# Kernel optimization log

Measured on AMD Instinct MI355X. Metric: run time of the kernel, lower is better.

The kernel has to match this reference:

```python
import jax, jax.numpy as jnp
import numpy as np

N_U = 50000
N_I = 50000
E = 800000
E_LBL = 200000
D_IN = 128
HID = 256
OUT = 128


def setup_inputs() -> dict:
    key = jax.random.key(0)
    ks = jax.random.split(key, 32)
    def glorot(k, shp):
        fan = shp[0] + shp[1]
        return jax.random.uniform(k, shp, jnp.float32, -1.0, 1.0) * np.sqrt(6.0 / fan)
    inp = {
        'x_user': jax.random.normal(ks[0], (N_U, D_IN), jnp.float32),
        'x_item': jax.random.normal(ks[1], (N_I, D_IN), jnp.float32),
        'edge_ui': jax.random.randint(ks[2], (2, E), 0, N_U, jnp.int32),
        'edge_iu': jax.random.randint(ks[3], (2, E), 0, N_I, jnp.int32),
        'edge_lbl': jax.random.randint(ks[4], (2, E_LBL), 0, N_U, jnp.int32),
        # layer 0 SAGE params (src_dim=D_IN, dst_dim=D_IN)
        'w_msg_ui0': glorot(ks[5], (D_IN, HID)), 'b_ui0': jnp.zeros((HID,), jnp.float32), 'w_root_ui0': glorot(ks[6], (D_IN, HID)),
        'w_msg_iu0': glorot(ks[7], (D_IN, HID)), 'b_iu0': jnp.zeros((HID,), jnp.float32), 'w_root_iu0': glorot(ks[8], (D_IN, HID)),
        # layer 1 SAGE params (src_dim=HID, dst_dim=HID)
        'w_msg_ui1': glorot(ks[9], (HID, HID)), 'b_ui1': jnp.zeros((HID,), jnp.float32), 'w_root_ui1': glorot(ks[10], (HID, HID)),
        'w_msg_iu1': glorot(ks[11], (HID, HID)), 'b_iu1': jnp.zeros((HID,), jnp.float32), 'w_root_iu1': glorot(ks[12], (HID, HID)),
        # per-node-type output linears on JK concat (2*HID -> OUT)
        'w_lin_u': glorot(ks[13], (2 * HID, OUT)), 'b_lin_u': jnp.zeros((OUT,), jnp.float32),
        'w_lin_i': glorot(ks[14], (2 * HID, OUT)), 'b_lin_i': jnp.zeros((OUT,), jnp.float32),
    }
    return inp


def _sage(x_src, x_dst, edge, w_msg, b_msg, w_root):
    # PyG SAGEConv(aggr='mean'): lin_l(mean_{j in N(i)} x_src[j]) + lin_r(x_dst[i])
    src, dst = edge[0], edge[1]
    n_dst = x_dst.shape[0]
    agg = jax.ops.segment_sum(x_src[src], dst, num_segments=n_dst)          # [n_dst, d_src]
    cnt = jax.ops.segment_sum(jnp.ones((edge.shape[1],), x_src.dtype), dst, num_segments=n_dst)
    mean = agg / jnp.maximum(cnt, 1.0)[:, None]
    return mean @ w_msg + b_msg + x_dst @ w_root


def reference(x_user, x_item, edge_ui, edge_iu, edge_lbl,
              w_msg_ui0, b_ui0, w_root_ui0, w_msg_iu0, b_iu0, w_root_iu0,
              w_msg_ui1, b_ui1, w_root_ui1, w_msg_iu1, b_iu1, w_root_iu1,
              w_lin_u, b_lin_u, w_lin_i, b_lin_i):
    # ----- encode: 2 HeteroConv(SAGEConv) layers -----
    item0 = _sage(x_user, x_item, edge_ui, w_msg_ui0, b_ui0, w_root_ui0)    # user->item
    user0 = _sage(x_item, x_user, edge_iu, b_msg=b_iu0, w_msg=w_msg_iu0, x_src=None, x_dst=None, edge=None, w_root=None) if False else _sage(x_item, x_user, edge_iu, w_msg_iu0, b_iu0, w_root_iu0)  # item->user
    item1 = _sage(user0, item0, edge_ui, w_msg_ui1, b_ui1, w_root_ui1)
    user1 = _sage(item0, user0, edge_iu, w_msg_iu1, b_iu1, w_root_iu1)
    # ----- JumpingKnowledge 'cat' + per-node-type linear -----
    z_user = jnp.concatenate([user0, user1], axis=-1) @ w_lin_u + b_lin_u   # [N_U, OUT]
    z_item = jnp.concatenate([item0, item1], axis=-1) @ w_lin_i + b_lin_i   # [N_I, OUT]
    # ----- decode: dot product over candidate edges (user, buys, item) -----
    pred = jnp.sum(z_user[edge_lbl[0]] * z_item[edge_lbl[1]], axis=-1)      # [E_LBL]
    return pred
```

## Files before the change

kernel.cpp:

```cpp
#include <hip/hip_runtime.h>

#define NU 50000
#define NI 50000
#define NE 800000
#define NLBL 200000
#define DIN 128
#define HID 256
#define DOUT 128

#define NSLICE 64
#define SLICE_SZ 12500
#define HALF_N 25000

typedef unsigned short ushort_t;
typedef __attribute__((ext_vector_type(8))) short bf16x8;
typedef __attribute__((ext_vector_type(4))) float f32x4;

__device__ __forceinline__ float bf2f(unsigned int u_shifted) {
    union { unsigned int i; float f; } v;
    v.i = u_shifted;
    return v.f;
}
__device__ __forceinline__ float bf_lo(unsigned int u) { return bf2f(u << 16); }
__device__ __forceinline__ float bf_hi(unsigned int u) { return bf2f(u & 0xffff0000u); }
__device__ __forceinline__ ushort_t f2bf(float f) {
    union { float f; unsigned int i; } v;
    v.f = f;
    unsigned int r = (v.i + 0x7FFFu + ((v.i >> 16) & 1u)) >> 16;
    return (ushort_t)r;
}
__device__ __forceinline__ void load_lds16(const ushort_t* g, ushort_t* s) {
    __builtin_amdgcn_global_load_lds(
        (const __attribute__((address_space(1))) void*)g,
        (__attribute__((address_space(3))) void*)s, 16, 0, 0);
}

#define CVT_PER 782
#define CVT_B (2 * CVT_PER)
#define SA_B 512

struct PrepArgs {
    const float* xu; ushort_t* xbu; const float* xi; ushort_t* xbi;
    const float *wm_ui1, *wr_ui1, *wm_iu1, *wr_iu1, *lin_i, *lin_u;
    float *G_i, *S_i, *G_u, *S_u;
};

__global__ __launch_bounds__(256) void prep_kernel(PrepArgs a) {
    int b = blockIdx.x;
    int t = threadIdx.x;
    if (b < CVT_B) {
        int cb = b;
        int which = (cb >= CVT_PER);
        if (which) cb -= CVT_PER;
        const float4* in = (const float4*)(which ? a.xi : a.xu);
        uint2* outp = (uint2*)(which ? a.xbi : a.xbu);
        const int n4 = NU * DIN / 4;
#pragma unroll
        for (int k = 0; k < 8; ++k) {
            int i = cb * 2048 + k * 256 + t;
            if (i < n4) {
                float4 v = in[i];
                uint2 o;
                o.x = (unsigned int)f2bf(v.x) | ((unsigned int)f2bf(v.y) << 16);
                o.y = (unsigned int)f2bf(v.z) | ((unsigned int)f2bf(v.w) << 16);
                outp[i] = o;
            }
        }
    } else {
        int r2 = b - CVT_B;
        int which = r2 >> 7;
        int e = (r2 & 127) * 256 + t;
        int k = e >> 7, n = e & 127;
        const float* W = (which == 0) ? a.wm_ui1 : (which == 1) ? a.wr_ui1
                       : (which == 2) ? a.wm_iu1 : a.wr_iu1;
        const float* L = (which < 2) ? a.lin_i : a.lin_u;
        float* O = (which == 0) ? a.G_i : (which == 1) ? a.S_i
                 : (which == 2) ? a.G_u : a.S_u;
        float s = (which & 1) ? L[k * 128 + n] : 0.f;
#pragma unroll 4
        for (int j = 0; j < HID; ++j) s += W[k * HID + j] * L[(HID + j) * 128 + n];
        O[k * 128 + n] = s;
    }
}

struct Prep2Args {
    const float *wm_ui0, *wr_ui0, *wm_iu0, *wr_iu0;
    const float *G_i, *S_i, *G_u, *S_u;
    const float *b_ui0, *b_iu0, *b_ui1, *b_iu1, *lin_i, *lin_u, *bl_i, *bl_u;
    ushort_t *VT1_i, *VT2_i, *VT3_i, *VT1_u, *VT2_u, *VT3_u;
    float *bz_i, *bz_u;
};

__global__ __launch_bounds__(256) void prep2_kernel(Prep2Args a) {
    int b = blockIdx.x, t = threadIdx.x;
    if (b < 384) {
        int v = b >> 6;
        int e = (b & 63) * 256 + t;
        int k = e >> 7, n = e & 127;
        const float *A1, *X1, *A2 = nullptr, *X2 = nullptr;
        ushort_t* O;
        switch (v) {
            case 0: A1 = a.wm_ui0; X1 = a.S_i; A2 = a.wr_iu0; X2 = a.G_i; O = a.VT1_i; break;
            case 1: A1 = a.wr_ui0; X1 = a.S_i; O = a.VT2_i; break;
            case 2: A1 = a.wm_iu0; X1 = a.G_i; O = a.VT3_i; break;
            case 3: A1 = a.wm_iu0; X1 = a.S_u; A2 = a.wr_ui0; X2 = a.G_u; O = a.VT1_u; break;
            case 4: A1 = a.wr_iu0; X1 = a.S_u; O = a.VT2_u; break;
            default: A1 = a.wm_ui0; X1 = a.G_u; O = a.VT3_u; break;
        }
        float s = 0.f;
#pragma unroll 4
        for (int j = 0; j < HID; ++j) s += A1[k * HID + j] * X1[j * 128 + n];
        if (A2) {
#pragma unroll 4
            for (int j = 0; j < HID; ++j) s += A2[k * HID + j] * X2[j * 128 + n];
        }
        O[n * 128 + k] = f2bf(s);
    } else {
        if (t >= 128) return;
        int user = b - 384;
        int n = t;
        const float* S = user ? a.S_u : a.S_i;
        const float* G = user ? a.G_u : a.G_i;
        const float* b_own0 = user ? a.b_iu0 : a.b_ui0;
        const float* b_oth0 = user ? a.b_ui0 : a.b_iu0;
        const float* b_own1 = user ? a.b_iu1 : a.b_ui1;
        const float* lin = user ? a.lin_u : a.lin_i;
        const float* bl = user ? a.bl_u : a.bl_i;
        float* o = user ? a.bz_u : a.bz_i;
        float s = bl[n];
        for (int j = 0; j < HID; ++j)
            s += b_own0[j] * S[j * 128 + n] + b_oth0[j] * G[j * 128 + n] +
                 b_own1[j] * lin[(HID + j) * 128 + n];
        o[n] = s;
    }
}

__global__ __launch_bounds__(256) void hist_lds(const int* __restrict__ dui,
                                                const int* __restrict__ diu,
                                                ushort_t* __restrict__ cnt_s) {
    __shared__ unsigned int cnt[HALF_N / 2];
    int b = blockIdx.x, t = threadIdx.x;
    int g = b >> 7, s = (b >> 1) & 63, half = b & 1;
    for (int i = t; i < HALF_N / 2; i += 256) cnt[i] = 0;
    __syncthreads();
    const int* dst = g ? diu : dui;
    int hbase = half * HALF_N;
    int e0 = s * SLICE_SZ;
    for (int i = e0 + t; i < e0 + SLICE_SZ; i += 256) {
        int d = dst[i] - hbase;
        if ((unsigned)d < (unsigned)HALF_N)
            atomicAdd(&cnt[d >> 1], 1u << ((d & 1) * 16));
    }
    __syncthreads();
    unsigned int* outp = (unsigned int*)(cnt_s + ((size_t)(g * NSLICE + s)) * 50000 + hbase);
    for (int i = t; i < HALF_N / 2; i += 256) outp[i] = cnt[i];
}

__global__ __launch_bounds__(256) void sscan(ushort_t* __restrict__ cnt_s, int* __restrict__ totals) {
    int idx = blockIdx.x * 256 + threadIdx.x;
    if (idx == 0) totals[100000] = 2 * NE;
    if (idx >= 100000) return;
    int g = idx / 50000, node = idx - g * 50000;
    size_t base = (size_t)g * NSLICE * 50000 + node;
    int run = 0;
#pragma unroll 4
    for (int s = 0; s < NSLICE; ++s) {
        size_t o = base + (size_t)s * 50000;
        int c = cnt_s[o];
        cnt_s[o] = (ushort_t)run;
        run += c;
    }
    totals[idx] = run;
}

__global__ __launch_bounds__(256) void scan1(const int* __restrict__ d, int* __restrict__ part, int n) {
    __shared__ int wsum[4];
    int b = blockIdx.x, t = threadIdx.x;
    int i0 = b * 2048 + t * 8;
    int s = 0;
#pragma unroll
    for (int k = 0; k < 8; ++k) s += (i0 + k < n) ? d[i0 + k] : 0;
#pragma unroll
    for (int off = 32; off > 0; off >>= 1) s += __shfl_down(s, off, 64);
    if ((t & 63) == 0) wsum[t >> 6] = s;
    __syncthreads();
    if (t == 0) part[b] = wsum[0] + wsum[1] + wsum[2] + wsum[3];
}

__global__ __launch_bounds__(256) void scan3(int* __restrict__ d, const int* __restrict__ part,
                                             int n, int nb) {
    __shared__ int wsum[4];
    __shared__ int blockoff_sh;
    int b = blockIdx.x, t = threadIdx.x;
    int lane = t & 63, wv = t >> 6;
    if (t < 64) {
        int v = (t < nb) ? part[t] : 0;
        int incl = v;
#pragma unroll
        for (int off = 1; off < 64; off <<= 1) {
            int tv = __shfl_up(incl, off, 64);
            if (t >= off) incl += tv;
        }
        if (t == b) blockoff_sh = incl - v;
    }
    int i0 = b * 2048 + t * 8;
    int v[8];
    int tsum = 0;
#pragma unroll
    for (int k = 0; k < 8; ++k) {
        v[k] = (i0 + k < n) ? d[i0 + k] : 0;
        tsum += v[k];
    }
    int incl = tsum;
#pragma unroll
    for (int off = 1; off < 64; off <<= 1) {
        int tv = __shfl_up(incl, off, 64);
        if (lane >= off) incl += tv;
    }
    if (lane == 63) wsum[wv] = incl;
    __syncthreads();
    int woff = 0;
    for (int w = 0; w < wv; ++w) woff += wsum[w];
    int run = blockoff_sh + woff + (incl - tsum);
#pragma unroll
    for (int k = 0; k < 8; ++k) {
        if (i0 + k < n) d[i0 + k] = run;
        run += v[k];
    }
}

__global__ __launch_bounds__(256) void fill_lds(const int* __restrict__ eui,
                                                const int* __restrict__ eiu,
                                                const ushort_t* __restrict__ cnt_s,
                                                const int* __restrict__ rowstart,
                                                ushort_t* __restrict__ csr) {
    __shared__ unsigned int off[HALF_N / 2];
    int b = blockIdx.x, t = threadIdx.x;
    int g = b >> 7, s = (b >> 1) & 63, half = b & 1;
    const unsigned int* st =
        (const unsigned int*)(cnt_s + ((size_t)(g * NSLICE + s)) * 50000 + half * HALF_N);
    for (int i = t; i < HALF_N / 2; i += 256) off[i] = st[i];
    __syncthreads();
    const int* src = g ? eiu : eui;
    const int* dst = src + NE;
    const int* rs = rowstart + g * 50000;
    int hbase = half * HALF_N;
    int e0 = s * SLICE_SZ;
    for (int i = e0 + t; i < e0 + SLICE_SZ; i += 256) {
        int dd = dst[i];
        int d = dd - hbase;
        if ((unsigned)d < (unsigned)HALF_N) {
            unsigned old = atomicAdd(&off[d >> 1], 1u << ((d & 1) * 16));
            int rel = (int)((old >> ((d & 1) * 16)) & 0xffffu);
            csr[(size_t)rs[dd] + rel] = (ushort_t)src[i];
        }
    }
}

struct AggJob { const int* sp; const ushort_t* csr; const ushort_t* x; ushort_t* out; int n; };
struct AggJobs2 { AggJob j[2]; };

__global__ __launch_bounds__(256) void agg_din(AggJobs2 js) {
    AggJob jb = js.j[blockIdx.y];
    int wave = (int)((blockIdx.x * 256u + threadIdx.x) >> 6);
    int lane = threadIdx.x & 63;
    const int l = lane & 15;
    const int h = lane >> 4;
    int w4 = wave * 4;
    if (w4 >= jb.n) return;
    int w = w4 + h;
    int s0 = jb.sp[w];
    int s1 = jb.sp[w + 1];
    int cnt = s1 - s0;
    float sc = (cnt > 0) ? 1.0f / (float)cnt : 0.0f;
    int cmax = cnt;
    {
        int c1 = __shfl_xor(cmax, 16, 64); cmax = (cmax > c1) ? cmax : c1;
        int c2 = __shfl_xor(cmax, 32, 64); cmax = (cmax > c2) ? cmax : c2;
    }
    const uint4* xp = (const uint4*)jb.x;
    float f0 = 0.f, f1 = 0.f, f2 = 0.f, f3 = 0.f;
    float f4 = 0.f, f5 = 0.f, f6 = 0.f, f7 = 0.f;
#define ACC8(m, u)                                                     \
    f0 = fmaf(m, bf_lo(u.x), f0); f1 = fmaf(m, bf_hi(u.x), f1);        \
    f2 = fmaf(m, bf_lo(u.y), f2); f3 = fmaf(m, bf_hi(u.y), f3);        \
    f4 = fmaf(m, bf_lo(u.z), f4); f5 = fmaf(m, bf_hi(u.z), f5);        \
    f6 = fmaf(m, bf_lo(u.w), f6); f7 = fmaf(m, bf_hi(u.w), f7);
    for (int chunk = 0; chunk < cmax; chunk += 16) {
        int mh = cnt - chunk;
        int safe = (mh > 0) ? ((l < mh) ? l : mh - 1) : 0;
        int vidx = (int)jb.csr[s0 + chunk + safe];
        int mm = cmax - chunk;
        if (mm > 16) mm = 16;
        int j = 0;
        for (; j + 3 < mm; j += 4) {
            int i0 = __shfl(vidx, j, 16);
            int i1 = __shfl(vidx, j + 1, 16);
            int i2 = __shfl(vidx, j + 2, 16);
            int i3 = __shfl(vidx, j + 3, 16);
            float m0 = (j < mh) ? 1.f : 0.f;
            float m1 = (j + 1 < mh) ? 1.f : 0.f;
            float m2 = (j + 2 < mh) ? 1.f : 0.f;
            float m3 = (j + 3 < mh) ? 1.f : 0.f;
            uint4 u0 = xp[(size_t)((j < mh) ? i0 : 0) * 16 + l];
            uint4 u1 = xp[(size_t)((j + 1 < mh) ? i1 : 0) * 16 + l];
            uint4 u2 = xp[(size_t)((j + 2 < mh) ? i2 : 0) * 16 + l];
            uint4 u3 = xp[(size_t)((j + 3 < mh) ? i3 : 0) * 16 + l];
            ACC8(m0, u0);
            ACC8(m1, u1);
            ACC8(m2, u2);
            ACC8(m3, u3);
        }
        for (; j < mm; ++j) {
            int i0 = __shfl(vidx, j, 16);
            float m0 = (j < mh) ? 1.f : 0.f;
            uint4 u0 = xp[(size_t)((j < mh) ? i0 : 0) * 16 + l];
            ACC8(m0, u0);
        }
    }
#undef ACC8
    uint4 o;
    o.x = (unsigned int)f2bf(f0 * sc) | ((unsigned int)f2bf(f1 * sc) << 16);
    o.y = (unsigned int)f2bf(f2 * sc) | ((unsigned int)f2bf(f3 * sc) << 16);
    o.z = (unsigned int)f2bf(f4 * sc) | ((unsigned int)f2bf(f5 * sc) << 16);
    o.w = (unsigned int)f2bf(f6 * sc) | ((unsigned int)f2bf(f7 * sc) << 16);
    ((uint4*)jb.out)[(size_t)w * 16 + l] = o;
}

struct GemmJob {
    const ushort_t* A[3];
    const ushort_t* WT[3];
    int K[3];
    const float* bias;
    void* C;
};
struct GemmJobs2 { GemmJob j[2]; };

template <int NP, typename OutT>
__global__ __launch_bounds__(256) void gemmN(GemmJobs2 js, int M, int N) {
    GemmJob jb = js.j[blockIdx.z];
    __shared__ ushort_t sA[128 * 32];
    __shared__ ushort_t sB[128 * 32];
    const int tid = threadIdx.x;
    const int lane = tid & 63;
    const int wv = tid >> 6;
    const int wm = wv & 1, wn = wv >> 1;
    const int bm = blockIdx.y * 128, bn = blockIdx.x * 128;

    f32x4 acc[4][4] = {};

    const int srow = tid >> 2;
    const int scol = (tid & 3) * 8;

#pragma unroll
    for (int part = 0; part < NP; ++part) {
        const ushort_t* A = jb.A[part];
        const ushort_t* WT = jb.WT[part];
        const int K = jb.K[part];
        int ar0 = bm + srow;       if (ar0 > M - 1) ar0 = M - 1;
        int ar1 = bm + 64 + srow;  if (ar1 > M - 1) ar1 = M - 1;
        const size_t aoff0 = (size_t)ar0 * K + scol;
        const size_t aoff1 = (size_t)ar1 * K + scol;
        const size_t boff0 = (size_t)(bn + srow) * K + scol;
        const size_t boff1 = (size_t)(bn + 64 + srow) * K + scol;
        for (int k0 = 0; k0 < K; k0 += 32) {
            __syncthreads();
            load_lds16(A + aoff0 + k0, sA + tid * 8);
            load_lds16(A + aoff1 + k0, sA + 2048 + tid * 8);
            load_lds16(WT + boff0 + k0, sB + tid * 8);
            load_lds16(WT + boff1 + k0, sB + 2048 + tid * 8);
            __syncthreads();
            const ushort_t* pA = sA + ((wm * 64 + (lane & 15)) * 32 + (lane >> 4) * 8);
            const ushort_t* pB = sB + ((wn * 64 + (lane & 15)) * 32 + (lane >> 4) * 8);
            bf16x8 af[4], bfr[4];
#pragma unroll
            for (int mt = 0; mt < 4; ++mt) af[mt] = *(const bf16x8*)(pA + mt * 512);
#pragma unroll
            for (int nt = 0; nt < 4; ++nt) bfr[nt] = *(const bf16x8*)(pB + nt * 512);
#pragma unroll
            for (int mt = 0; mt < 4; ++mt)
#pragma unroll
                for (int nt = 0; nt < 4; ++nt)
                    acc[mt][nt] = __builtin_amdgcn_mfma_f32_16x16x32_bf16(
                        af[mt], bfr[nt], acc[mt][nt], 0, 0, 0);
        }
    }

#pragma unroll
    for (int mt = 0; mt < 4; ++mt) {
#pragma unroll
        for (int r = 0; r < 4; ++r) {
            int row = bm + wm * 64 + mt * 16 + (lane >> 4) * 4 + r;
            if (row >= M) continue;
#pragma unroll
            for (int nt = 0; nt < 4; ++nt) {
                int col = bn + wn * 64 + nt * 16 + (lane & 15);
                float v = acc[mt][nt][r] + jb.bias[col];
                if constexpr (sizeof(OutT) == 2)
                    ((ushort_t*)jb.C)[(size_t)row * N + col] = f2bf(v);
                else
                    ((float*)jb.C)[(size_t)row * N + col] = v;
            }
        }
    }
}

__global__ void decode_kernel(const int* __restrict__ lbl, const ushort_t* __restrict__ zu,
                              const ushort_t* __restrict__ zi, float* __restrict__ out, int n) {
    int gid = blockIdx.x * blockDim.x + threadIdx.x;
    int wave = gid >> 6;
    int lane = threadIdx.x & 63;
    int q = lane >> 4;
    int l = lane & 15;
    int e = wave * 4 + q;
    if (e >= n) return;
    int u = lbl[e];
    int it = lbl[n + e];
    uint4 a = ((const uint4*)zu)[(size_t)u * 16 + l];
    uint4 b = ((const uint4*)zi)[(size_t)it * 16 + l];
    float s = bf_lo(a.x) * bf_lo(b.x) + bf_hi(a.x) * bf_hi(b.x) +
              bf_lo(a.y) * bf_lo(b.y) + bf_hi(a.y) * bf_hi(b.y) +
              bf_lo(a.z) * bf_lo(b.z) + bf_hi(a.z) * bf_hi(b.z) +
              bf_lo(a.w) * bf_lo(b.w) + bf_hi(a.w) * bf_hi(b.w);
#pragma unroll
    for (int off = 8; off > 0; off >>= 1) s += __shfl_down(s, off, 16);
    if (l == 0) out[e] = s;
}

extern "C" void kernel_launch(void* const* d_in, const int* in_sizes, int n_in,
                              void* d_out, int out_size, void* d_ws, size_t ws_size,
                              hipStream_t stream) {
    const float* x_user = (const float*)d_in[0];
    const float* x_item = (const float*)d_in[1];
    const int* edge_ui = (const int*)d_in[2];
    const int* edge_iu = (const int*)d_in[3];
    const int* edge_lbl = (const int*)d_in[4];
    const float* w_msg_ui0 = (const float*)d_in[5];
    const float* b_ui0 = (const float*)d_in[6];
    const float* w_root_ui0 = (const float*)d_in[7];
    const float* w_msg_iu0 = (const float*)d_in[8];
    const float* b_iu0 = (const float*)d_in[9];
    const float* w_root_iu0 = (const float*)d_in[10];
    const float* w_msg_ui1 = (const float*)d_in[11];
    const float* b_ui1 = (const float*)d_in[12];
    const float* w_root_ui1 = (const float*)d_in[13];
    const float* w_msg_iu1 = (const float*)d_in[14];
    const float* b_iu1 = (const float*)d_in[15];
    const float* w_root_iu1 = (const float*)d_in[16];
    const float* w_lin_u = (const float*)d_in[17];
    const float* b_lin_u = (const float*)d_in[18];
    const float* w_lin_i = (const float*)d_in[19];
    const float* b_lin_i = (const float*)d_in[20];
    float* out = (float*)d_out;

    char* p = (char*)d_ws;
    ushort_t* user0 = (ushort_t*)p;  p += (size_t)NU * HID * 2;
    ushort_t* item0 = (ushort_t*)p;  p += (size_t)NI * HID * 2;
    ushort_t* user1 = (ushort_t*)p;  p += (size_t)NU * HID * 2;
    ushort_t* item1 = (ushort_t*)p;  p += (size_t)NI * HID * 2;
    (void)user0; (void)item0; (void)user1; (void)item1;
    ushort_t* A_i  = (ushort_t*)p;   p += (size_t)NI * DIN * 2;
    ushort_t* A_u  = (ushort_t*)p;   p += (size_t)NU * DIN * 2;
    ushort_t* B_i  = (ushort_t*)p;   p += (size_t)NI * DIN * 2;
    ushort_t* B_u  = (ushort_t*)p;   p += (size_t)NU * DIN * 2;
    ushort_t* xb_u  = (ushort_t*)p;  p += (size_t)NU * DIN * 2;
    ushort_t* xb_i  = (ushort_t*)p;  p += (size_t)NI * DIN * 2;
    ushort_t* z_user = (ushort_t*)p; p += (size_t)NU * DOUT * 2;
    ushort_t* z_item = (ushort_t*)p; p += (size_t)NI * DOUT * 2;
    int* totals     = (int*)p;       p += (size_t)(100000 + 64) * 4;
    ushort_t* csr   = (ushort_t*)p;  p += (size_t)2 * NE * 2;
    ushort_t* cnt_s = (ushort_t*)p;  p += (size_t)2 * NSLICE * 50000 * 2;
    int* scan_part  = (int*)p;       p += 64 * 4;
    float* G_i = (float*)p; p += (size_t)HID * 128 * 4;
    float* S_i = (float*)p; p += (size_t)HID * 128 * 4;
    float* G_u = (float*)p; p += (size_t)HID * 128 * 4;
    float* S_u = (float*)p; p += (size_t)HID * 128 * 4;
    ushort_t* VT1_i = (ushort_t*)p; p += (size_t)128 * 128 * 2;
    ushort_t* VT2_i = (ushort_t*)p; p += (size_t)128 * 128 * 2;
    ushort_t* VT3_i = (ushort_t*)p; p += (size_t)128 * 128 * 2;
    ushort_t* VT1_u = (ushort_t*)p; p += (size_t)128 * 128 * 2;
    ushort_t* VT2_u = (ushort_t*)p; p += (size_t)128 * 128 * 2;
    ushort_t* VT3_u = (ushort_t*)p; p += (size_t)128 * 128 * 2;
    float* bz_i = (float*)p; p += 128 * 4;
    float* bz_u = (float*)p; p += 128 * 4;

    const int NCNT = 100000;
    const int NB = (NCNT + 2047) / 2048;

    PrepArgs pa;
    pa.xu = x_user; pa.xbu = xb_u; pa.xi = x_item; pa.xbi = xb_i;
    pa.wm_ui1 = w_msg_ui1; pa.wr_ui1 = w_root_ui1;
    pa.wm_iu1 = w_msg_iu1; pa.wr_iu1 = w_root_iu1;
    pa.lin_i = w_lin_i; pa.lin_u = w_lin_u;
    pa.G_i = G_i; pa.S_i = S_i; pa.G_u = G_u; pa.S_u = S_u;
    prep_kernel<<<CVT_B + SA_B, 256, 0, stream>>>(pa);

    Prep2Args p2;
    p2.wm_ui0 = w_msg_ui0; p2.wr_ui0 = w_root_ui0;
    p2.wm_iu0 = w_msg_iu0; p2.wr_iu0 = w_root_iu0;
    p2.G_i = G_i; p2.S_i = S_i; p2.G_u = G_u; p2.S_u = S_u;
    p2.b_ui0 = b_ui0; p2.b_iu0 = b_iu0; p2.b_ui1 = b_ui1; p2.b_iu1 = b_iu1;
    p2.lin_i = w_lin_i; p2.lin_u = w_lin_u; p2.bl_i = b_lin_i; p2.bl_u = b_lin_u;
    p2.VT1_i = VT1_i; p2.VT2_i = VT2_i; p2.VT3_i = VT3_i;
    p2.VT1_u = VT1_u; p2.VT2_u = VT2_u; p2.VT3_u = VT3_u;
    p2.bz_i = bz_i; p2.bz_u = bz_u;
    prep2_kernel<<<386, 256, 0, stream>>>(p2);

    hist_lds<<<256, 256, 0, stream>>>(edge_ui + NE, edge_iu + NE, cnt_s);
    sscan<<<(NCNT + 255) / 256 + 1, 256, 0, stream>>>(cnt_s, totals);
    scan1<<<NB, 256, 0, stream>>>(totals, scan_part, NCNT);
    scan3<<<NB, 256, 0, stream>>>(totals, scan_part, NCNT, NB);
    fill_lds<<<256, 256, 0, stream>>>(edge_ui, edge_iu, cnt_s, totals, csr);

    {
        AggJobs2 aj = {{{totals, csr, xb_u, A_i, NI},
                        {totals + 50000, csr, xb_i, A_u, NU}}};
        agg_din<<<dim3((NI / 4 * 64) / 256, 2), 256, 0, stream>>>(aj);
    }
    {
        AggJobs2 aj = {{{totals, csr, A_u, B_i, NI},
                        {totals + 50000, csr, A_i, B_u, NU}}};
        agg_din<<<dim3((NI / 4 * 64) / 256, 2), 256, 0, stream>>>(aj);
    }

    {
        GemmJobs2 gj = {{{{A_i, xb_i, B_i}, {VT1_i, VT2_i, VT3_i}, {DIN, DIN, DIN}, bz_i, z_item},
                         {{A_u, xb_u, B_u}, {VT1_u, VT2_u, VT3_u}, {DIN, DIN, DIN}, bz_u, z_user}}};
        gemmN<3, ushort_t><<<dim3(DOUT / 128, (NU + 127) / 128, 2), 256, 0, stream>>>(gj, NU, DOUT);
    }

    decode_kernel<<<(((NLBL + 3) / 4) * 64 + 255) / 256, 256, 0, stream>>>(
        edge_lbl, z_user, z_item, out, NLBL);
}
```

Before: 397.5 us.

## Fuse prep stages with histogram/scan and split aggregation across feature halves

Restructures the front-end launches. Weight-precompute work is merged into the histogram kernel and the second prep into the per-slice scan kernel, and the separate block-sum scan kernel is replaced by atomic accumulation into zeroed partials. This cuts launch count and lets independent small jobs overlap. The aggregation kernel now splits each 128-wide bf16 row into two 64-wide halves across a new grid dimension, doubling wave count with 8-byte loads instead of 16-byte. That adds parallelism but repeats the CSR index reads per half.

After: 372.5 us. -6.3%, faster.

```diff
diff --git a/kernel.cpp b/kernel.cpp
--- a/kernel.cpp
+++ b/kernel.cpp
@@ -39,35 +39,59 @@
 #define CVT_B (2 * CVT_PER)
 #define SA_B 512
 
-struct PrepArgs {
+struct CvtArgs {
     const float* xu; ushort_t* xbu; const float* xi; ushort_t* xbi;
+};
+
+__global__ __launch_bounds__(256) void cvt_kernel(CvtArgs a) {
+    int b = blockIdx.x;
+    int t = threadIdx.x;
+    int which = (b >= CVT_PER);
+    int cb = which ? b - CVT_PER : b;
+    const float4* in = (const float4*)(which ? a.xi : a.xu);
+    uint2* outp = (uint2*)(which ? a.xbi : a.xbu);
+    const int n4 = NU * DIN / 4;
+#pragma unroll
+    for (int k = 0; k < 8; ++k) {
+        int i = cb * 2048 + k * 256 + t;
+        if (i < n4) {
+            float4 v = in[i];
+            uint2 o;
+            o.x = (unsigned int)f2bf(v.x) | ((unsigned int)f2bf(v.y) << 16);
+            o.y = (unsigned int)f2bf(v.z) | ((unsigned int)f2bf(v.w) << 16);
+            outp[i] = o;
+        }
+    }
+}
+
+struct HistSaArgs {
+    const int *eui, *eiu;
+    ushort_t* cnt_s;
     const float *wm_ui1, *wr_ui1, *wm_iu1, *wr_iu1, *lin_i, *lin_u;
     float *G_i, *S_i, *G_u, *S_u;
+    int* scan_part;
 };
 
-__global__ __launch_bounds__(256) void prep_kernel(PrepArgs a) {
-    int b = blockIdx.x;
-    int t = threadIdx.x;
-    if (b < CVT_B) {
-        int cb = b;
-        int which = (cb >= CVT_PER);
-        if (which) cb -= CVT_PER;
-        const float4* in = (const float4*)(which ? a.xi : a.xu);
-        uint2* outp = (uint2*)(which ? a.xbi : a.xbu);
-        const int n4 = NU * DIN / 4;
-#pragma unroll
-        for (int k = 0; k < 8; ++k) {
-            int i = cb * 2048 + k * 256 + t;
-            if (i < n4) {
-                float4 v = in[i];
-                uint2 o;
-                o.x = (unsigned int)f2bf(v.x) | ((unsigned int)f2bf(v.y) << 16);
-                o.y = (unsigned int)f2bf(v.z) | ((unsigned int)f2bf(v.w) << 16);
-                outp[i] = o;
-            }
-        }
-    } else {
-        int r2 = b - CVT_B;
+__global__ __launch_bounds__(256) void hist_sa(HistSaArgs a) {
+    __shared__ unsigned int cnt[HALF_N / 2];
+    int b = blockIdx.x, t = threadIdx.x;
+    if (b < 256) {
+        int g = b >> 7, s = (b >> 1) & 63, half = b & 1;
+        for (int i = t; i < HALF_N / 2; i += 256) cnt[i] = 0;
+        __syncthreads();
+        const int* dst = (g ? a.eiu : a.eui) + NE;
+        int hbase = half * HALF_N;
+        int e0 = s * SLICE_SZ;
+        for (int i = e0 + t; i < e0 + SLICE_SZ; i += 256) {
+            int d = dst[i] - hbase;
+            if ((unsigned)d < (unsigned)HALF_N)
+                atomicAdd(&cnt[d >> 1], 1u << ((d & 1) * 16));
+        }
+        __syncthreads();
+        unsigned int* outp = (unsigned int*)(a.cnt_s + ((size_t)(g * NSLICE + s)) * 50000 + hbase);
+        for (int i = t; i < HALF_N / 2; i += 256) outp[i] = cnt[i];
+    } else if (b < 256 + SA_B) {
+        int r2 = b - 256;
         int which = r2 >> 7;
         int e = (r2 & 127) * 256 + t;
         int k = e >> 7, n = e & 127;
@@ -80,10 +104,15 @@
 #pragma unroll 4
         for (int j = 0; j < HID; ++j) s += W[k * HID + j] * L[(HID + j) * 128 + n];
         O[k * 128 + n] = s;
-    }
-}
-
-struct Prep2Args {
+    } else {
+        if (t < 64) a.scan_part[t] = 0;
+    }
+}
+
+struct SscanP2Args {
+    ushort_t* cnt_s;
+    int* totals;
+    int* scan_part;
     const float *wm_ui0, *wr_ui0, *wm_iu0, *wr_iu0;
     const float *G_i, *S_i, *G_u, *S_u;
     const float *b_ui0, *b_iu0, *b_ui1, *b_iu1, *lin_i, *lin_u, *bl_i, *bl_u;
@@ -91,100 +120,73 @@
     float *bz_i, *bz_u;
 };
 
-__global__ __launch_bounds__(256) void prep2_kernel(Prep2Args a) {
-    int b = blockIdx.x, t = threadIdx.x;
-    if (b < 384) {
-        int v = b >> 6;
-        int e = (b & 63) * 256 + t;
-        int k = e >> 7, n = e & 127;
-        const float *A1, *X1, *A2 = nullptr, *X2 = nullptr;
-        ushort_t* O;
-        switch (v) {
-            case 0: A1 = a.wm_ui0; X1 = a.S_i; A2 = a.wr_iu0; X2 = a.G_i; O = a.VT1_i; break;
-            case 1: A1 = a.wr_ui0; X1 = a.S_i; O = a.VT2_i; break;
-            case 2: A1 = a.wm_iu0; X1 = a.G_i; O = a.VT3_i; break;
-            case 3: A1 = a.wm_iu0; X1 = a.S_u; A2 = a.wr_ui0; X2 = a.G_u; O = a.VT1_u; break;
-            case 4: A1 = a.wr_iu0; X1 = a.S_u; O = a.VT2_u; break;
-            default: A1 = a.wm_ui0; X1 = a.G_u; O = a.VT3_u; break;
-        }
-        float s = 0.f;
-#pragma unroll 4
-        for (int j = 0; j < HID; ++j) s += A1[k * HID + j] * X1[j * 128 + n];
-        if (A2) {
-#pragma unroll 4
-            for (int j = 0; j < HID; ++j) s += A2[k * HID + j] * X2[j * 128 + n];
-        }
-        O[n * 128 + k] = f2bf(s);
-    } else {
-        if (t >= 128) return;
-        int user = b - 384;
-        int n = t;
-        const float* S = user ? a.S_u : a.S_i;
-        const float* G = user ? a.G_u : a.G_i;
-        const float* b_own0 = user ? a.b_iu0 : a.b_ui0;
-        const float* b_oth0 = user ? a.b_ui0 : a.b_iu0;
-        const float* b_own1 = user ? a.b_iu1 : a.b_ui1;
-        const float* lin = user ? a.lin_u : a.lin_i;
-        const float* bl = user ? a.bl_u : a.bl_i;
-        float* o = user ? a.bz_u : a.bz_i;
-        float s = bl[n];
-        for (int j = 0; j < HID; ++j)
-            s += b_own0[j] * S[j * 128 + n] + b_oth0[j] * G[j * 128 + n] +
-                 b_own1[j] * lin[(HID + j) * 128 + n];
-        o[n] = s;
-    }
-}
-
-__global__ __launch_bounds__(256) void hist_lds(const int* __restrict__ dui,
-                                                const int* __restrict__ diu,
-                                                ushort_t* __restrict__ cnt_s) {
-    __shared__ unsigned int cnt[HALF_N / 2];
-    int b = blockIdx.x, t = threadIdx.x;
-    int g = b >> 7, s = (b >> 1) & 63, half = b & 1;
-    for (int i = t; i < HALF_N / 2; i += 256) cnt[i] = 0;
-    __syncthreads();
-    const int* dst = g ? diu : dui;
-    int hbase = half * HALF_N;
-    int e0 = s * SLICE_SZ;
-    for (int i = e0 + t; i < e0 + SLICE_SZ; i += 256) {
-        int d = dst[i] - hbase;
-        if ((unsigned)d < (unsigned)HALF_N)
-            atomicAdd(&cnt[d >> 1], 1u << ((d & 1) * 16));
-    }
-    __syncthreads();
-    unsigned int* outp = (unsigned int*)(cnt_s + ((size_t)(g * NSLICE + s)) * 50000 + hbase);
-    for (int i = t; i < HALF_N / 2; i += 256) outp[i] = cnt[i];
-}
-
-__global__ __launch_bounds__(256) void sscan(ushort_t* __restrict__ cnt_s, int* __restrict__ totals) {
-    int idx = blockIdx.x * 256 + threadIdx.x;
-    if (idx == 0) totals[100000] = 2 * NE;
-    if (idx >= 100000) return;
-    int g = idx / 50000, node = idx - g * 50000;
-    size_t base = (size_t)g * NSLICE * 50000 + node;
-    int run = 0;
-#pragma unroll 4
-    for (int s = 0; s < NSLICE; ++s) {
-        size_t o = base + (size_t)s * 50000;
-        int c = cnt_s[o];
-        cnt_s[o] = (ushort_t)run;
-        run += c;
-    }
-    totals[idx] = run;
-}
-
-__global__ __launch_bounds__(256) void scan1(const int* __restrict__ d, int* __restrict__ part, int n) {
+__global__ __launch_bounds__(256) void sscan_prep2(SscanP2Args a) {
     __shared__ int wsum[4];
     int b = blockIdx.x, t = threadIdx.x;
-    int i0 = b * 2048 + t * 8;
-    int s = 0;
-#pragma unroll
-    for (int k = 0; k < 8; ++k) s += (i0 + k < n) ? d[i0 + k] : 0;
-#pragma unroll
-    for (int off = 32; off > 0; off >>= 1) s += __shfl_down(s, off, 64);
-    if ((t & 63) == 0) wsum[t >> 6] = s;
-    __syncthreads();
-    if (t == 0) part[b] = wsum[0] + wsum[1] + wsum[2] + wsum[3];
+    if (b < 392) {
+        if (b == 0 && t == 0) a.totals[100000] = 2 * NE;
+        int idx = b * 256 + t;
+        int run = 0;
+        if (idx < 100000) {
+            int g = idx / 50000, node = idx - g * 50000;
+            size_t base = (size_t)g * NSLICE * 50000 + node;
+#pragma unroll 4
+            for (int s = 0; s < NSLICE; ++s) {
+                size_t o = base + (size_t)s * 50000;
+                int c = a.cnt_s[o];
+                a.cnt_s[o] = (ushort_t)run;
+                run += c;
+            }
+            a.totals[idx] = run;
+        }
+        int s = run;
+#pragma unroll
+        for (int off = 32; off > 0; off >>= 1) s += __shfl_down(s, off, 64);
+        if ((t & 63) == 0) wsum[t >> 6] = s;
+        __syncthreads();
+        if (t == 0) atomicAdd(&a.scan_part[b >> 3], wsum[0] + wsum[1] + wsum[2] + wsum[3]);
+    } else {
+        int task = b - 392;
+        if (task < 384) {
+            int v = task >> 6;
+            int e = (task & 63) * 256 + t;
+            int k = e >> 7, n = e & 127;
+            const float *A1, *X1, *A2 = nullptr, *X2 = nullptr;
+            ushort_t* O;
+            switch (v) {
+                case 0: A1 = a.wm_ui0; X1 = a.S_i; A2 = a.wr_iu0; X2 = a.G_i; O = a.VT1_i; break;
+                case 1: A1 = a.wr_ui0; X1 = a.S_i; O = a.VT2_i; break;
+                case 2: A1 = a.wm_iu0; X1 = a.G_i; O = a.VT3_i; break;
+                case 3: A1 = a.wm_iu0; X1 = a.S_u; A2 = a.wr_ui0; X2 = a.G_u; O = a.VT1_u; break;
+                case 4: A1 = a.wr_iu0; X1 = a.S_u; O = a.VT2_u; break;
+                default: A1 = a.wm_ui0; X1 = a.G_u; O = a.VT3_u; break;
+            }
+            float s = 0.f;
+#pragma unroll 4
+            for (int j = 0; j < HID; ++j) s += A1[k * HID + j] * X1[j * 128 + n];
+            if (A2) {
+#pragma unroll 4
+                for (int j = 0; j < HID; ++j) s += A2[k * HID + j] * X2[j * 128 + n];
+            }
+            O[n * 128 + k] = f2bf(s);
+        } else if (t < 128) {
+            int user = task - 384;
+            int n = t;
+            const float* S = user ? a.S_u : a.S_i;
+            const float* G = user ? a.G_u : a.G_i;
+            const float* b_own0 = user ? a.b_iu0 : a.b_ui0;
+            const float* b_oth0 = user ? a.b_ui0 : a.b_iu0;
+            const float* b_own1 = user ? a.b_iu1 : a.b_ui1;
+            const float* lin = user ? a.lin_u : a.lin_i;
+            const float* bl = user ? a.bl_u : a.bl_i;
+            float* o = user ? a.bz_u : a.bz_i;
+            float s = bl[n];
+            for (int j = 0; j < HID; ++j)
+                s += b_own0[j] * S[j * 128 + n] + b_oth0[j] * G[j * 128 + n] +
+                     b_own1[j] * lin[(HID + j) * 128 + n];
+            o[n] = s;
+        }
+    }
 }
 
 __global__ __launch_bounds__(256) void scan3(int* __restrict__ d, const int* __restrict__ part,
@@ -262,6 +264,7 @@
 
 __global__ __launch_bounds__(256) void agg_din(AggJobs2 js) {
     AggJob jb = js.j[blockIdx.y];
+    const int half = blockIdx.z;
     int wave = (int)((blockIdx.x * 256u + threadIdx.x) >> 6);
     int lane = threadIdx.x & 63;
     const int l = lane & 15;
@@ -278,14 +281,11 @@
         int c1 = __shfl_xor(cmax, 16, 64); cmax = (cmax > c1) ? cmax : c1;
         int c2 = __shfl_xor(cmax, 32, 64); cmax = (cmax > c2) ? cmax : c2;
     }
-    const uint4* xp = (const uint4*)jb.x;
+    const uint2* xp = (const uint2*)jb.x + half * 16;
     float f0 = 0.f, f1 = 0.f, f2 = 0.f, f3 = 0.f;
-    float f4 = 0.f, f5 = 0.f, f6 = 0.f, f7 = 0.f;
-#define ACC8(m, u)                                                     \
+#define ACC4(m, u)                                                     \
     f0 = fmaf(m, bf_lo(u.x), f0); f1 = fmaf(m, bf_hi(u.x), f1);        \
-    f2 = fmaf(m, bf_lo(u.y), f2); f3 = fmaf(m, bf_hi(u.y), f3);        \
-    f4 = fmaf(m, bf_lo(u.z), f4); f5 = fmaf(m, bf_hi(u.z), f5);        \
-    f6 = fmaf(m, bf_lo(u.w), f6); f7 = fmaf(m, bf_hi(u.w), f7);
+    f2 = fmaf(m, bf_lo(u.y), f2); f3 = fmaf(m, bf_hi(u.y), f3);
     for (int chunk = 0; chunk < cmax; chunk += 16) {
         int mh = cnt - chunk;
         int safe = (mh > 0) ? ((l < mh) ? l : mh - 1) : 0;
@@ -302,29 +302,27 @@
             float m1 = (j + 1 < mh) ? 1.f : 0.f;
             float m2 = (j + 2 < mh) ? 1.f : 0.f;
             float m3 = (j + 3 < mh) ? 1.f : 0.f;
-            uint4 u0 = xp[(size_t)((j < mh) ? i0 : 0) * 16 + l];
-            uint4 u1 = xp[(size_t)((j + 1 < mh) ? i1 : 0) * 16 + l];
-            uint4 u2 = xp[(size_t)((j + 2 < mh) ? i2 : 0) * 16 + l];
-            uint4 u3 = xp[(size_t)((j + 3 < mh) ? i3 : 0) * 16 + l];
-            ACC8(m0, u0);
-            ACC8(m1, u1);
-            ACC8(m2, u2);
-            ACC8(m3, u3);
+            uint2 u0 = xp[(size_t)((j < mh) ? i0 : 0) * 32 + l];
+            uint2 u1 = xp[(size_t)((j + 1 < mh) ? i1 : 0) * 32 + l];
+            uint2 u2 = xp[(size_t)((j + 2 < mh) ? i2 : 0) * 32 + l];
+            uint2 u3 = xp[(size_t)((j + 3 < mh) ? i3 : 0) * 32 + l];
+            ACC4(m0, u0);
+            ACC4(m1, u1);
+            ACC4(m2, u2);
+            ACC4(m3, u3);
         }
         for (; j < mm; ++j) {
             int i0 = __shfl(vidx, j, 16);
             float m0 = (j < mh) ? 1.f : 0.f;
-            uint4 u0 = xp[(size_t)((j < mh) ? i0 : 0) * 16 + l];
-            ACC8(m0, u0);
-        }
-    }
-#undef ACC8
-    uint4 o;
+            uint2 u0 = xp[(size_t)((j < mh) ? i0 : 0) * 32 + l];
+            ACC4(m0, u0);
+        }
+    }
+#undef ACC4
+    uint2 o;
     o.x = (unsigned int)f2bf(f0 * sc) | ((unsigned int)f2bf(f1 * sc) << 16);
     o.y = (unsigned int)f2bf(f2 * sc) | ((unsigned int)f2bf(f3 * sc) << 16);
-    o.z = (unsigned int)f2bf(f4 * sc) | ((unsigned int)f2bf(f5 * sc) << 16);
-    o.w = (unsigned int)f2bf(f6 * sc) | ((unsigned int)f2bf(f7 * sc) << 16);
-    ((uint4*)jb.out)[(size_t)w * 16 + l] = o;
+    ((uint2*)jb.out)[(size_t)w * 32 + half * 16 + l] = o;
 }
 
 struct GemmJob {
@@ -487,40 +485,43 @@
     const int NCNT = 100000;
     const int NB = (NCNT + 2047) / 2048;
 
-    PrepArgs pa;
-    pa.xu = x_user; pa.xbu = xb_u; pa.xi = x_item; pa.xbi = xb_i;
-    pa.wm_ui1 = w_msg_ui1; pa.wr_ui1 = w_root_ui1;
-    pa.wm_iu1 = w_msg_iu1; pa.wr_iu1 = w_root_iu1;
-    pa.lin_i = w_lin_i; pa.lin_u = w_lin_u;
-    pa.G_i = G_i; pa.S_i = S_i; pa.G_u = G_u; pa.S_u = S_u;
-    prep_kernel<<<CVT_B + SA_B, 256, 0, stream>>>(pa);
-
-    Prep2Args p2;
-    p2.wm_ui0 = w_msg_ui0; p2.wr_ui0 = w_root_ui0;
-    p2.wm_iu0 = w_msg_iu0; p2.wr_iu0 = w_root_iu0;
-    p2.G_i = G_i; p2.S_i = S_i; p2.G_u = G_u; p2.S_u = S_u;
-    p2.b_ui0 = b_ui0; p2.b_iu0 = b_iu0; p2.b_ui1 = b_ui1; p2.b_iu1 = b_iu1;
-    p2.lin_i = w_lin_i; p2.lin_u = w_lin_u; p2.bl_i = b_lin_i; p2.bl_u = b_lin_u;
-    p2.VT1_i = VT1_i; p2.VT2_i = VT2_i; p2.VT3_i = VT3_i;
-    p2.VT1_u = VT1_u; p2.VT2_u = VT2_u; p2.VT3_u = VT3_u;
-    p2.bz_i = bz_i; p2.bz_u = bz_u;
-    prep2_kernel<<<386, 256, 0, stream>>>(p2);
-
-    hist_lds<<<256, 256, 0, stream>>>(edge_ui + NE, edge_iu + NE, cnt_s);
-    sscan<<<(NCNT + 255) / 256 + 1, 256, 0, stream>>>(cnt_s, totals);
-    scan1<<<NB, 256, 0, stream>>>(totals, scan_part, NCNT);
+    CvtArgs cv = { x_user, xb_u, x_item, xb_i };
+    cvt_kernel<<<CVT_B, 256, 0, stream>>>(cv);
+
+    HistSaArgs hs;
+    hs.eui = edge_ui; hs.eiu = edge_iu; hs.cnt_s = cnt_s;
+    hs.wm_ui1 = w_msg_ui1; hs.wr_ui1 = w_root_ui1;
+    hs.wm_iu1 = w_msg_iu1; hs.wr_iu1 = w_root_iu1;
+    hs.lin_i = w_lin_i; hs.lin_u = w_lin_u;
+    hs.G_i = G_i; hs.S_i = S_i; hs.G_u = G_u; hs.S_u = S_u;
+    hs.scan_part = scan_part;
+    hist_sa<<<256 + SA_B + 1, 256, 0, stream>>>(hs);
+
+    SscanP2Args sp;
+    sp.cnt_s = cnt_s; sp.totals = totals; sp.scan_part = scan_part;
+    sp.wm_ui0 = w_msg_ui0; sp.wr_ui0 = w_root_ui0;
+    sp.wm_iu0 = w_msg_iu0; sp.wr_iu0 = w_root_iu0;
+    sp.G_i = G_i; sp.S_i = S_i; sp.G_u = G_u; sp.S_u = S_u;
+    sp.b_ui0 = b_ui0; sp.b_iu0 = b_iu0; sp.b_ui1 = b_ui1; sp.b_iu1 = b_iu1;
+    sp.lin_i = w_lin_i; sp.lin_u = w_lin_u; sp.bl_i = b_lin_i; sp.bl_u = b_lin_u;
+    sp.VT1_i = VT1_i; sp.VT2_i = VT2_i; sp.VT3_i = VT3_i;
+    sp.VT1_u = VT1_u; sp.VT2_u = VT2_u; sp.VT3_u = VT3_u;
+    sp.bz_i = bz_i; sp.bz_u = bz_u;
+    sscan_prep2<<<392 + 386, 256, 0, stream>>>(sp);
+
     scan3<<<NB, 256, 0, stream>>>(totals, scan_part, NCNT, NB);
+
     fill_lds<<<256, 256, 0, stream>>>(edge_ui, edge_iu, cnt_s, totals, csr);
 
     {
         AggJobs2 aj = {{{totals, csr, xb_u, A_i, NI},
                         {totals + 50000, csr, xb_i, A_u, NU}}};
-        agg_din<<<dim3((NI / 4 * 64) / 256, 2), 256, 0, stream>>>(aj);
+        agg_din<<<dim3(3125, 2, 2), 256, 0, stream>>>(aj);
     }
     {
         AggJobs2 aj = {{{totals, csr, A_u, B_i, NI},
                         {totals + 50000, csr, A_i, B_u, NU}}};
-        agg_din<<<dim3((NI / 4 * 64) / 256, 2), 256, 0, stream>>>(aj);
+        agg_din<<<dim3(3125, 2, 2), 256, 0, stream>>>(aj);
     }
 
     {
```
